# Kernel tuning notes

Measured on AMD Instinct MI355X. Metric: run time of the kernel, lower is better.

The kernel has to match this reference:

```python
import jax, jax.numpy as jnp
import numpy as np

N_NODES = 100000
N_EDGES = 3200000
IN_CH = 512
HID_CH = 40   # 2 * out_channels
OUT_CH = 20


def setup_inputs() -> dict:
    key = jax.random.key(0)
    k1, k2, k3, k4, k5, k6 = jax.random.split(key, 6)
    x = jax.random.normal(k1, (N_NODES, IN_CH), dtype=jnp.float32)
    edge_index = jax.random.randint(k2, (2, N_EDGES), 0, N_NODES, dtype=jnp.int32)
    # Glorot-style init for GCN weights, zero bias (PyG default)
    W1 = jax.random.normal(k3, (IN_CH, HID_CH), dtype=jnp.float32) * (1.0 / np.sqrt(IN_CH))
    b1 = jnp.zeros((HID_CH,), dtype=jnp.float32)
    W2 = jax.random.normal(k4, (HID_CH, OUT_CH), dtype=jnp.float32) * (1.0 / np.sqrt(HID_CH))
    b2 = jnp.zeros((OUT_CH,), dtype=jnp.float32)
    return {"x": x, "edge_index": edge_index, "W1": W1, "b1": b1, "W2": W2, "b2": b2}


def _gcn_conv(x, src, dst, W, b):
    """PyG GCNConv: add self-loops, symmetric norm, linear, scatter-add, bias."""
    n = x.shape[0]
    loops = jnp.arange(n, dtype=src.dtype)
    src = jnp.concatenate([src, loops])
    dst = jnp.concatenate([dst, loops])
    # in-degree over A + I (self-loops guarantee deg >= 1)
    deg = jax.ops.segment_sum(jnp.ones(src.shape[0], x.dtype), dst, num_segments=n)
    dinv = jax.lax.rsqrt(deg)
    norm = dinv[src] * dinv[dst]               # [E+N]
    h = x @ W                                   # [N, out] GEMM before aggregation
    msg = h[src] * norm[:, None]                # gather + scale
    out = jax.ops.segment_sum(msg, dst, num_segments=n)  # scatter-add at targets
    return out + b


def reference(x, edge_index, W1, b1, W2, b2):
    src, dst = edge_index[0], edge_index[1]
    h = jax.nn.relu(_gcn_conv(x, src, dst, W1, b1))
    # dropout is identity in eval mode (training=False)
    return _gcn_conv(h, src, dst, W2, b2)
```

## Files before the change

kernel.cpp:

```cpp
#include <hip/hip_runtime.h>
#include <cstddef>

static constexpr int NN   = 100000;
static constexpr int NE   = 3200000;
static constexpr int CIN  = 512;
static constexpr int CHID = 40;
static constexpr int COUT = 20;

typedef float f32x4 __attribute__((ext_vector_type(4)));


__global__ __launch_bounds__(256) void k_count(const int* __restrict__ dst, int* __restrict__ cnt,
                                               int* __restrict__ rank, int n_edges4) {
  const int e4 = blockIdx.x * 256 + threadIdx.x;
  if (e4 >= n_edges4) return;
  const int4 d = ((const int4*)dst)[e4];
  int4 r;
  r.x = atomicAdd(&cnt[d.x], 1);
  r.y = atomicAdd(&cnt[d.y], 1);
  r.z = atomicAdd(&cnt[d.z], 1);
  r.w = atomicAdd(&cnt[d.w], 1);
  ((int4*)rank)[e4] = r;
}

__global__ __launch_bounds__(256) void k_scanA(const int* __restrict__ cnt, int* __restrict__ excl,
                                               int* __restrict__ bsums, float* __restrict__ dinv, int n) {
  __shared__ int sdata[256];
  const int t = threadIdx.x;
  const int base = blockIdx.x * 1024 + t * 4;
  int v[4];
#pragma unroll
  for (int j = 0; j < 4; ++j) {
    const int i = base + j;
    v[j] = (i < n) ? cnt[i] : 0;
    if (i < n) dinv[i] = rsqrtf((float)(v[j] + 1));
  }
  const int s4 = v[0] + v[1] + v[2] + v[3];
  sdata[t] = s4;
  __syncthreads();
  for (int off = 1; off < 256; off <<= 1) {
    int val = 0;
    if (t >= off) val = sdata[t - off];
    __syncthreads();
    sdata[t] += val;
    __syncthreads();
  }
  int run = sdata[t] - s4;
#pragma unroll
  for (int j = 0; j < 4; ++j) {
    const int i = base + j;
    if (i < n) excl[i] = run;
    run += v[j];
  }
  if (t == 255) bsums[blockIdx.x] = sdata[255];
}

__global__ __launch_bounds__(256) void k_scanB(int* __restrict__ bsums, int nb) {
  __shared__ int sdata[256];
  const int t = threadIdx.x;
  const int v = (t < nb) ? bsums[t] : 0;
  sdata[t] = v;
  __syncthreads();
  for (int off = 1; off < 256; off <<= 1) {
    int val = 0;
    if (t >= off) val = sdata[t - off];
    __syncthreads();
    sdata[t] += val;
    __syncthreads();
  }
  if (t < nb) bsums[t] = sdata[t] - v;
}

__global__ __launch_bounds__(256) void k_scanC(int* __restrict__ rowptr, const int* __restrict__ boff,
                                               int n, int n_edges) {
  const int i = blockIdx.x * 256 + threadIdx.x;
  if (i < n) rowptr[i] += boff[i >> 10];
  if (i == 0) rowptr[n] = n_edges;
}

__global__ __launch_bounds__(256) void k_fill(const int* __restrict__ src, const int* __restrict__ dst,
                                              const int* __restrict__ rank, const int* __restrict__ rowptr,
                                              int* __restrict__ csr_src, int n_edges4) {
  const int e4 = blockIdx.x * 256 + threadIdx.x;
  if (e4 >= n_edges4) return;
  const int4 s = ((const int4*)src)[e4];
  const int4 d = ((const int4*)dst)[e4];
  const int4 r = ((const int4*)rank)[e4];
  csr_src[rowptr[d.x] + r.x] = s.x;
  csr_src[rowptr[d.y] + r.y] = s.y;
  csr_src[rowptr[d.z] + r.z] = s.z;
  csr_src[rowptr[d.w] + r.w] = s.w;
}

__global__ __launch_bounds__(256) void k_gemm1(const float* __restrict__ x, const float* __restrict__ W,
                                               float* __restrict__ h, int n) {
  __shared__ float xt[64 * 128];
  const int t  = threadIdx.x;
  const int nd = t & 63;
  const int g  = __builtin_amdgcn_readfirstlane(t >> 6);
  const int block0 = blockIdx.x * 64;

  const int sn = t >> 5;
  const int c4 = t & 31;

  float acc[10];
#pragma unroll
  for (int j = 0; j < 10; ++j) acc[j] = 0.f;

  for (int kt = 0; kt < 4; ++kt) {
    f32x4 v[8];
#pragma unroll
    for (int r = 0; r < 8; ++r) {
      const int row = r * 8 + sn;
      int gn = block0 + row;
      if (gn >= n) gn = n - 1;
      v[r] = __builtin_nontemporal_load(
          ((const f32x4*)(x + (size_t)gn * CIN + kt * 128)) + c4);
    }
    if (kt) __syncthreads();
#pragma unroll
    for (int r = 0; r < 8; ++r) {
      const int row = r * 8 + sn;
      const int byte = row * 512 + ((c4 * 16) ^ ((row & 31) << 4));
      *(f32x4*)((char*)xt + byte) = v[r];
    }
    __syncthreads();

    const float* __restrict__ Wg = W + (size_t)kt * 128 * CHID + g * 10;
#pragma unroll 4
    for (int k4 = 0; k4 < 32; ++k4) {
      const int byte = nd * 512 + ((k4 * 16) ^ ((nd & 31) << 4));
      const f32x4 xv = *(const f32x4*)((const char*)xt + byte);
      const float* __restrict__ Wk = Wg + k4 * 4 * CHID;
#pragma unroll
      for (int j = 0; j < 10; ++j) acc[j] = fmaf(xv.x, Wk[j], acc[j]);
#pragma unroll
      for (int j = 0; j < 10; ++j) acc[j] = fmaf(xv.y, Wk[CHID + j], acc[j]);
#pragma unroll
      for (int j = 0; j < 10; ++j) acc[j] = fmaf(xv.z, Wk[2 * CHID + j], acc[j]);
#pragma unroll
      for (int j = 0; j < 10; ++j) acc[j] = fmaf(xv.w, Wk[3 * CHID + j], acc[j]);
    }
  }

  __syncthreads();
#pragma unroll
  for (int j = 0; j < 10; ++j) xt[nd * 44 + g * 10 + j] = acc[j];
  __syncthreads();
  for (int i = t; i < 640; i += 256) {
    const int row = i / 10;
    const int c   = i % 10;
    const int node = block0 + row;
    if (node < n)
      ((float4*)(h + (size_t)node * CHID))[c] = *(const float4*)&xt[row * 44 + c * 4];
  }
}

__global__ __launch_bounds__(256) void k_gemm2(const float* __restrict__ t1, const float* __restrict__ W,
                                               float* __restrict__ g, int n) {
  const int node = blockIdx.x * 256 + threadIdx.x;
  if (node >= n) return;
  const float4* __restrict__ r4 = (const float4*)(t1 + (size_t)node * CHID);
  float acc[COUT];
#pragma unroll
  for (int c = 0; c < COUT; ++c) acc[c] = 0.f;
#pragma unroll
  for (int kk = 0; kk < CHID / 4; ++kk) {
    const float4 xv = r4[kk];
    const float* __restrict__ Wk = W + kk * 4 * COUT;
#pragma unroll
    for (int c = 0; c < COUT; ++c) {
      float a = acc[c];
      a = fmaf(xv.x, Wk[c], a);
      a = fmaf(xv.y, Wk[COUT + c], a);
      a = fmaf(xv.z, Wk[2 * COUT + c], a);
      a = fmaf(xv.w, Wk[3 * COUT + c], a);
      acc[c] = a;
    }
  }
  float* __restrict__ o = g + (size_t)node * COUT;
#pragma unroll
  for (int c = 0; c < COUT; ++c) o[c] = acc[c];
}

__global__ __launch_bounds__(256) void k_agg40(const float* __restrict__ h, const int* __restrict__ rowptr,
                                               const int* __restrict__ csr_src, const float* __restrict__ dinv,
                                               const float* __restrict__ bias, float* __restrict__ out, int n) {
  const int wave = (blockIdx.x * 256 + (int)threadIdx.x) >> 6;
  const int lane = threadIdx.x & 63;
  const int sub  = lane / 20;
  const int cp   = lane % 20;
  const int node = wave * 3 + sub;
  if (sub >= 3 || node >= n) return;
  const float2* __restrict__ h2 = (const float2*)h;
  const int r0 = rowptr[node];
  const int r1 = rowptr[node + 1];
  const float dv = dinv[node];
  const float self_w = dv * dv;
  float2 acc = h2[(size_t)node * 20 + cp];
  acc.x *= self_w;
  acc.y *= self_w;
  int i = r0;
  for (; i + 4 <= r1; i += 4) {
    const int s0 = csr_src[i + 0];
    const int s1 = csr_src[i + 1];
    const int s2 = csr_src[i + 2];
    const int s3 = csr_src[i + 3];
    const float w0 = dinv[s0] * dv;
    const float w1 = dinv[s1] * dv;
    const float w2 = dinv[s2] * dv;
    const float w3 = dinv[s3] * dv;
    const float2 g0 = h2[(size_t)s0 * 20 + cp];
    const float2 g1 = h2[(size_t)s1 * 20 + cp];
    const float2 g2 = h2[(size_t)s2 * 20 + cp];
    const float2 g3 = h2[(size_t)s3 * 20 + cp];
    acc.x = fmaf(g0.x, w0, acc.x); acc.y = fmaf(g0.y, w0, acc.y);
    acc.x = fmaf(g1.x, w1, acc.x); acc.y = fmaf(g1.y, w1, acc.y);
    acc.x = fmaf(g2.x, w2, acc.x); acc.y = fmaf(g2.y, w2, acc.y);
    acc.x = fmaf(g3.x, w3, acc.x); acc.y = fmaf(g3.y, w3, acc.y);
  }
  for (; i < r1; ++i) {
    const int s = csr_src[i];
    const float w = dinv[s] * dv;
    const float2 g = h2[(size_t)s * 20 + cp];
    acc.x = fmaf(g.x, w, acc.x);
    acc.y = fmaf(g.y, w, acc.y);
  }
  const float2 bv = ((const float2*)bias)[cp];
  float2 v;
  v.x = fmaxf(acc.x + bv.x, 0.f);
  v.y = fmaxf(acc.y + bv.y, 0.f);
  ((float2*)out)[(size_t)node * 20 + cp] = v;
}

__global__ __launch_bounds__(256) void k_agg20(const float* __restrict__ h, const int* __restrict__ rowptr,
                                               const int* __restrict__ csr_src, const float* __restrict__ dinv,
                                               const float* __restrict__ bias, float* __restrict__ out, int n) {
  const int wave = (blockIdx.x * 256 + (int)threadIdx.x) >> 6;
  const int lane = threadIdx.x & 63;
  const int sub  = lane / 10;
  const int cp   = lane % 10;
  const int node = wave * 6 + sub;
  if (sub >= 6 || node >= n) return;
  const float2* __restrict__ h2 = (const float2*)h;
  const int r0 = rowptr[node];
  const int r1 = rowptr[node + 1];
  const float dv = dinv[node];
  const float self_w = dv * dv;
  float2 acc = h2[(size_t)node * 10 + cp];
  acc.x *= self_w;
  acc.y *= self_w;
  int i = r0;
  for (; i + 4 <= r1; i += 4) {
    const int s0 = csr_src[i + 0];
    const int s1 = csr_src[i + 1];
    const int s2 = csr_src[i + 2];
    const int s3 = csr_src[i + 3];
    const float w0 = dinv[s0] * dv;
    const float w1 = dinv[s1] * dv;
    const float w2 = dinv[s2] * dv;
    const float w3 = dinv[s3] * dv;
    const float2 g0 = h2[(size_t)s0 * 10 + cp];
    const float2 g1 = h2[(size_t)s1 * 10 + cp];
    const float2 g2 = h2[(size_t)s2 * 10 + cp];
    const float2 g3 = h2[(size_t)s3 * 10 + cp];
    acc.x = fmaf(g0.x, w0, acc.x); acc.y = fmaf(g0.y, w0, acc.y);
    acc.x = fmaf(g1.x, w1, acc.x); acc.y = fmaf(g1.y, w1, acc.y);
    acc.x = fmaf(g2.x, w2, acc.x); acc.y = fmaf(g2.y, w2, acc.y);
    acc.x = fmaf(g3.x, w3, acc.x); acc.y = fmaf(g3.y, w3, acc.y);
  }
  for (; i < r1; ++i) {
    const int s = csr_src[i];
    const float w = dinv[s] * dv;
    const float2 g = h2[(size_t)s * 10 + cp];
    acc.x = fmaf(g.x, w, acc.x);
    acc.y = fmaf(g.y, w, acc.y);
  }
  const float2 bv = ((const float2*)bias)[cp];
  float2 v;
  v.x = acc.x + bv.x;
  v.y = acc.y + bv.y;
  ((float2*)out)[(size_t)node * 10 + cp] = v;
}


extern "C" void kernel_launch(void* const* d_in, const int* in_sizes, int n_in,
                              void* d_out, int out_size, void* d_ws, size_t ws_size,
                              hipStream_t stream) {
  const float* x   = (const float*)d_in[0];
  const int*   ei  = (const int*)d_in[1];
  const float* W1  = (const float*)d_in[2];
  const float* b1  = (const float*)d_in[3];
  const float* W2  = (const float*)d_in[4];
  const float* b2  = (const float*)d_in[5];
  float* out = (float*)d_out;

  const int* srcp = ei;
  const int* dstp = ei + NE;

  char* ws = (char*)d_ws;
  size_t off = 0;
  auto take = [&](size_t bytes) -> char* {
    char* p = ws + off;
    off = (off + bytes + 255) & ~(size_t)255;
    return p;
  };
  int*   cnt     = (int*)take((size_t)NN * 4);
  int*   rowptr  = (int*)take((size_t)(NN + 1) * 4);
  float* dinv    = (float*)take((size_t)NN * 4);
  int*   bsums   = (int*)take(256 * 4);
  int*   rank    = (int*)take((size_t)NE * 4);
  int*   csr_src = (int*)take((size_t)NE * 4);
  float* h1      = (float*)take((size_t)NN * CHID * 4);
  float* t1      = (float*)take((size_t)NN * CHID * 4);
  float* g2      = h1;

  (void)in_sizes; (void)n_in; (void)out_size; (void)ws_size;

  hipMemsetAsync(cnt, 0, (size_t)NN * 4, stream);

  const int ne4 = NE / 4;
  k_count<<<(ne4 + 255) / 256, 256, 0, stream>>>(dstp, cnt, rank, ne4);
  const int nb = (NN + 1023) / 1024;
  k_scanA<<<nb, 256, 0, stream>>>(cnt, rowptr, bsums, dinv, NN);
  k_scanB<<<1, 256, 0, stream>>>(bsums, nb);
  k_scanC<<<(NN + 255) / 256, 256, 0, stream>>>(rowptr, bsums, NN, NE);
  k_fill<<<(ne4 + 255) / 256, 256, 0, stream>>>(srcp, dstp, rank, rowptr, csr_src, ne4);

  k_gemm1<<<(NN + 63) / 64, 256, 0, stream>>>(x, W1, h1, NN);
  const int nwaves1 = (NN + 2) / 3;
  k_agg40<<<(nwaves1 + 3) / 4, 256, 0, stream>>>(h1, rowptr, csr_src, dinv, b1, t1, NN);
  k_gemm2<<<(NN + 255) / 256, 256, 0, stream>>>(t1, W2, g2, NN);
  const int nwaves2 = (NN + 5) / 6;
  k_agg20<<<(nwaves2 + 3) / 4, 256, 0, stream>>>(g2, rowptr, csr_src, dinv, b2, out, NN);
}
```

Measured before the change: 764.1 us.

## Privatize degree counting per block and prefetch next GEMM1 K-tile into registers

Replaces the global-atomic in-degree count with 64 per-block private count arrays, using workgroup-scope atomics and a merge kernel that turns them into per-block offsets, which the fill kernel then adds when placing sources. The aim is to cut contention on global atomics. Separately, the first GEMM loads the next 128-wide K slice of x into registers while computing on the current one, hiding load latency. The privatized path needs a 25.6 MB workspace plus a 25.6 MB memset, and it only runs when the provided workspace is large enough.

After: 837.6 us. 9.6% more time.

```diff
diff --git a/kernel.cpp b/kernel.cpp
--- a/kernel.cpp
+++ b/kernel.cpp
@@ -6,9 +6,42 @@
 static constexpr int CIN  = 512;
 static constexpr int CHID = 40;
 static constexpr int COUT = 20;
+static constexpr int NB   = 64;
+static constexpr int CHUNK = NE / NB;
 
 typedef float f32x4 __attribute__((ext_vector_type(4)));
 
+
+__global__ __launch_bounds__(1024) void k_countP(const int* __restrict__ dst, int* __restrict__ cntb,
+                                                 int* __restrict__ rank) {
+  const int b = blockIdx.x;
+  int* __restrict__ cb = cntb + (size_t)b * NN;
+  const int base = b * (CHUNK / 4);
+  const int end  = base + CHUNK / 4;
+  for (int i = base + (int)threadIdx.x; i < end; i += 1024) {
+    const int4 d = ((const int4*)dst)[i];
+    int4 r;
+    r.x = __hip_atomic_fetch_add(&cb[d.x], 1, __ATOMIC_RELAXED, __HIP_MEMORY_SCOPE_WORKGROUP);
+    r.y = __hip_atomic_fetch_add(&cb[d.y], 1, __ATOMIC_RELAXED, __HIP_MEMORY_SCOPE_WORKGROUP);
+    r.z = __hip_atomic_fetch_add(&cb[d.z], 1, __ATOMIC_RELAXED, __HIP_MEMORY_SCOPE_WORKGROUP);
+    r.w = __hip_atomic_fetch_add(&cb[d.w], 1, __ATOMIC_RELAXED, __HIP_MEMORY_SCOPE_WORKGROUP);
+    ((int4*)rank)[i] = r;
+  }
+}
+
+__global__ __launch_bounds__(256) void k_merge(int* __restrict__ cntb, int* __restrict__ cnt, int n) {
+  const int i = blockIdx.x * 256 + threadIdx.x;
+  if (i >= n) return;
+  int s = 0;
+#pragma unroll 8
+  for (int b = 0; b < NB; ++b) {
+    int* p = cntb + (size_t)b * NN + i;
+    const int t = *p;
+    *p = s;
+    s += t;
+  }
+  cnt[i] = s;
+}
 
 __global__ __launch_bounds__(256) void k_count(const int* __restrict__ dst, int* __restrict__ cnt,
                                                int* __restrict__ rank, int n_edges4) {
@@ -78,6 +111,23 @@
   if (i == 0) rowptr[n] = n_edges;
 }
 
+__global__ __launch_bounds__(256) void k_fillP(const int* __restrict__ src, const int* __restrict__ dst,
+                                               const int* __restrict__ rank, const int* __restrict__ rowptr,
+                                               const int* __restrict__ cntb, int* __restrict__ csr_src,
+                                               int n_edges4) {
+  const int e4 = blockIdx.x * 256 + threadIdx.x;
+  if (e4 >= n_edges4) return;
+  const int4 s = ((const int4*)src)[e4];
+  const int4 d = ((const int4*)dst)[e4];
+  const int4 r = ((const int4*)rank)[e4];
+  const int b = (e4 * 4) / CHUNK;
+  const int* __restrict__ cb = cntb + (size_t)b * NN;
+  csr_src[rowptr[d.x] + cb[d.x] + r.x] = s.x;
+  csr_src[rowptr[d.y] + cb[d.y] + r.y] = s.y;
+  csr_src[rowptr[d.z] + cb[d.z] + r.z] = s.z;
+  csr_src[rowptr[d.w] + cb[d.w] + r.w] = s.w;
+}
+
 __global__ __launch_bounds__(256) void k_fill(const int* __restrict__ src, const int* __restrict__ dst,
                                               const int* __restrict__ rank, const int* __restrict__ rowptr,
                                               int* __restrict__ csr_src, int n_edges4) {
@@ -107,24 +157,33 @@
 #pragma unroll
   for (int j = 0; j < 10; ++j) acc[j] = 0.f;
 
+  f32x4 v[8];
+#pragma unroll
+  for (int r = 0; r < 8; ++r) {
+    const int row = r * 8 + sn;
+    int gn = block0 + row;
+    if (gn >= n) gn = n - 1;
+    v[r] = __builtin_nontemporal_load(((const f32x4*)(x + (size_t)gn * CIN)) + c4);
+  }
+#pragma unroll
+  for (int r = 0; r < 8; ++r) {
+    const int row = r * 8 + sn;
+    const int byte = row * 512 + ((c4 * 16) ^ ((row & 31) << 4));
+    *(f32x4*)((char*)xt + byte) = v[r];
+  }
+  __syncthreads();
+
   for (int kt = 0; kt < 4; ++kt) {
-    f32x4 v[8];
-#pragma unroll
-    for (int r = 0; r < 8; ++r) {
-      const int row = r * 8 + sn;
-      int gn = block0 + row;
-      if (gn >= n) gn = n - 1;
-      v[r] = __builtin_nontemporal_load(
-          ((const f32x4*)(x + (size_t)gn * CIN + kt * 128)) + c4);
+    if (kt < 3) {
+#pragma unroll
+      for (int r = 0; r < 8; ++r) {
+        const int row = r * 8 + sn;
+        int gn = block0 + row;
+        if (gn >= n) gn = n - 1;
+        v[r] = __builtin_nontemporal_load(
+            ((const f32x4*)(x + (size_t)gn * CIN + (kt + 1) * 128)) + c4);
+      }
     }
-    if (kt) __syncthreads();
-#pragma unroll
-    for (int r = 0; r < 8; ++r) {
-      const int row = r * 8 + sn;
-      const int byte = row * 512 + ((c4 * 16) ^ ((row & 31) << 4));
-      *(f32x4*)((char*)xt + byte) = v[r];
-    }
-    __syncthreads();
 
     const float* __restrict__ Wg = W + (size_t)kt * 128 * CHID + g * 10;
 #pragma unroll 4
@@ -140,6 +199,17 @@
       for (int j = 0; j < 10; ++j) acc[j] = fmaf(xv.z, Wk[2 * CHID + j], acc[j]);
 #pragma unroll
       for (int j = 0; j < 10; ++j) acc[j] = fmaf(xv.w, Wk[3 * CHID + j], acc[j]);
+    }
+
+    if (kt < 3) {
+      __syncthreads();
+#pragma unroll
+      for (int r = 0; r < 8; ++r) {
+        const int row = r * 8 + sn;
+        const int byte = row * 512 + ((c4 * 16) ^ ((row & 31) << 4));
+        *(f32x4*)((char*)xt + byte) = v[r];
+      }
+      __syncthreads();
     }
   }
 
@@ -314,18 +384,32 @@
   float* h1      = (float*)take((size_t)NN * CHID * 4);
   float* t1      = (float*)take((size_t)NN * CHID * 4);
   float* g2      = h1;
-
-  (void)in_sizes; (void)n_in; (void)out_size; (void)ws_size;
-
-  hipMemsetAsync(cnt, 0, (size_t)NN * 4, stream);
+  const size_t base_need = off;
+  int*   cntb    = (int*)take((size_t)NB * NN * 4);
+  const bool privatized = (ws_size >= off);
+
+  (void)in_sizes; (void)n_in; (void)out_size;
 
   const int ne4 = NE / 4;
-  k_count<<<(ne4 + 255) / 256, 256, 0, stream>>>(dstp, cnt, rank, ne4);
   const int nb = (NN + 1023) / 1024;
-  k_scanA<<<nb, 256, 0, stream>>>(cnt, rowptr, bsums, dinv, NN);
-  k_scanB<<<1, 256, 0, stream>>>(bsums, nb);
-  k_scanC<<<(NN + 255) / 256, 256, 0, stream>>>(rowptr, bsums, NN, NE);
-  k_fill<<<(ne4 + 255) / 256, 256, 0, stream>>>(srcp, dstp, rank, rowptr, csr_src, ne4);
+
+  if (privatized) {
+    hipMemsetAsync(cntb, 0, (size_t)NB * NN * 4, stream);
+    k_countP<<<NB, 1024, 0, stream>>>(dstp, cntb, rank);
+    k_merge<<<(NN + 255) / 256, 256, 0, stream>>>(cntb, cnt, NN);
+    k_scanA<<<nb, 256, 0, stream>>>(cnt, rowptr, bsums, dinv, NN);
+    k_scanB<<<1, 256, 0, stream>>>(bsums, nb);
+    k_scanC<<<(NN + 255) / 256, 256, 0, stream>>>(rowptr, bsums, NN, NE);
+    k_fillP<<<(ne4 + 255) / 256, 256, 0, stream>>>(srcp, dstp, rank, rowptr, cntb, csr_src, ne4);
+  } else {
+    hipMemsetAsync(cnt, 0, (size_t)NN * 4, stream);
+    k_count<<<(ne4 + 255) / 256, 256, 0, stream>>>(dstp, cnt, rank, ne4);
+    k_scanA<<<nb, 256, 0, stream>>>(cnt, rowptr, bsums, dinv, NN);
+    k_scanB<<<1, 256, 0, stream>>>(bsums, nb);
+    k_scanC<<<(NN + 255) / 256, 256, 0, stream>>>(rowptr, bsums, NN, NE);
+    k_fill<<<(ne4 + 255) / 256, 256, 0, stream>>>(srcp, dstp, rank, rowptr, csr_src, ne4);
+  }
+  (void)base_need;
 
   k_gemm1<<<(NN + 63) / 64, 256, 0, stream>>>(x, W1, h1, NN);
   const int nwaves1 = (NN + 2) / 3;
```
